# Performance work log

Hardware: AMD Instinct MI355X
Metric: run time of the kernel (lower is better)

## Reference

```python
import jax, jax.numpy as jnp
import numpy as np

NUM_HEADS = 16
HEAD_DIM = 80
DIM = NUM_HEADS * HEAD_DIM
SEQ = 2048
SCALE = HEAD_DIM ** -0.5


def rotate_half(x):
    x1, x2 = jnp.split(x, 2, axis=-1)
    return jnp.concatenate((-x2, x1), axis=-1)


def setup_inputs() -> dict:
    key = jax.random.key(0)
    ks = jax.random.split(key, 8)
    hidden_states = jax.random.normal(ks[0], (SEQ, DIM), dtype=jnp.float32)
    cu_seqlens = jnp.array([0, SEQ], dtype=jnp.int32)  # unused by the math
    # rotary embeddings for head_dim
    inv_freq = 1.0 / (10000.0 ** (jnp.arange(0, HEAD_DIM // 2, dtype=jnp.float32) / (HEAD_DIM // 2)))
    freqs = jnp.outer(jnp.arange(SEQ, dtype=jnp.float32), inv_freq)  # [S, hd/2]
    emb = jnp.concatenate((freqs, freqs), axis=-1)  # [S, hd]
    cos = jnp.cos(emb)
    sin = jnp.sin(emb)
    w_qkv = jax.random.normal(ks[1], (3 * DIM, DIM), dtype=jnp.float32) * (DIM ** -0.5)
    b_qkv = jax.random.normal(ks[2], (3 * DIM,), dtype=jnp.float32) * 0.02
    w_proj = jax.random.normal(ks[3], (DIM, DIM), dtype=jnp.float32) * (DIM ** -0.5)
    b_proj = jax.random.normal(ks[4], (DIM,), dtype=jnp.float32) * 0.02
    return {"hidden_states": hidden_states, "cu_seqlens": cu_seqlens, "cos": cos,
            "sin": sin, "w_qkv": w_qkv, "b_qkv": b_qkv, "w_proj": w_proj, "b_proj": b_proj}


def reference(hidden_states, cu_seqlens, cos, sin, w_qkv, b_qkv, w_proj, b_proj):
    S = hidden_states.shape[0]
    qkv = hidden_states @ w_qkv.T + b_qkv  # [S, 3*D]
    qkv = qkv.reshape(S, 3, NUM_HEADS, HEAD_DIM)
    q, k, v = qkv[:, 0], qkv[:, 1], qkv[:, 2]  # each [S, H, hd]
    c = cos[:, None, :]  # [S, 1, hd]
    s = sin[:, None, :]
    q = q * c + rotate_half(q) * s
    k = k * c + rotate_half(k) * s
    # SDPA, non-causal: [H, S, S]
    scores = jnp.einsum('shd,thd->hst', q, k) * SCALE
    attn = jax.nn.softmax(scores, axis=-1)
    out = jnp.einsum('hst,thd->shd', attn, v).reshape(S, DIM)
    return out @ w_proj.T + b_proj
```

## Files before the change

kernel.cpp:

```cpp
#include <hip/hip_runtime.h>


#define SEQLEN   2048
#define DIMM     1280
#define NHEADS   16
#define HD       80
#define HDP      96
#define QKV_N    3840
#define NSPLIT   4
#define KVSPAN   (SEQLEN / NSPLIT)
#define QSCALE_LOG2E 0.16130083587064776f

#define KSTRIDE  104
#define VFSTRIDE 24

#define EXP2F(x) __builtin_amdgcn_exp2f(x)

#define GLD16(gptr, lptr)                                                      \
    __builtin_amdgcn_global_load_lds(                                          \
        (const __attribute__((address_space(1))) void*)(gptr),                 \
        (__attribute__((address_space(3))) void*)(lptr), 16, 0, 0)

typedef float f32x4 __attribute__((ext_vector_type(4)));
typedef _Float16 half8 __attribute__((ext_vector_type(8)));
typedef _Float16 half4 __attribute__((ext_vector_type(4)));

static __device__ __forceinline__ f32x4 mfma_16x16x32(half8 a, half8 b, f32x4 c) {
    return __builtin_amdgcn_mfma_f32_16x16x32_f16(a, b, c, 0, 0, 0);
}
static __device__ __forceinline__ f32x4 mfma_16x16x16(half4 a, half4 b, f32x4 c) {
    return __builtin_amdgcn_mfma_f32_16x16x16f16(a, b, c, 0, 0, 0);
}
static __device__ __forceinline__ half4 lo4(half8 v) {
    return __builtin_shufflevector(v, v, 0, 1, 2, 3);
}
static __device__ __forceinline__ half4 hi4(half8 v) {
    return __builtin_shufflevector(v, v, 4, 5, 6, 7);
}

__global__ __launch_bounds__(256)
void cast_all(const float* __restrict__ hs, const float* __restrict__ wq,
              const float* __restrict__ wp, _Float16* __restrict__ dhs,
              _Float16* __restrict__ dwq, _Float16* __restrict__ dwp) {
    const int n1 = SEQLEN * DIMM / 4, n2 = QKV_N * DIMM / 4, n3 = DIMM * DIMM / 4;
    int i = blockIdx.x * 256 + threadIdx.x;
    const float4* src; half4* dst; int j;
    if (i < n1)           { src = (const float4*)hs; dst = (half4*)dhs; j = i; }
    else if (i < n1 + n2) { src = (const float4*)wq; dst = (half4*)dwq; j = i - n1; }
    else if (i < n1 + n2 + n3) { src = (const float4*)wp; dst = (half4*)dwp; j = i - n1 - n2; }
    else return;
    const float4 v = src[j];
    half4 h;
    h.x = (_Float16)v.x; h.y = (_Float16)v.y;
    h.z = (_Float16)v.z; h.w = (_Float16)v.w;
    dst[j] = h;
}

template<bool OUT_F16>
__global__ __launch_bounds__(256, 2)
void gemm_bt64(const _Float16* __restrict__ A, const _Float16* __restrict__ B,
               const float* __restrict__ bias, void* __restrict__ Cout,
               int M, int N, int K) {
    __shared__ __align__(16) _Float16 As[2][64 * 32];
    __shared__ __align__(16) _Float16 Bs[2][128 * 32];
    const int tid  = threadIdx.x;
    const int lane = tid & 63;
    const int wave = tid >> 6;
    const int l15  = lane & 15;
    const int quad = lane >> 4;
    const int wm   = wave & 1;
    const int wn   = wave >> 1;
    const long bm = blockIdx.x, bn = blockIdx.y;

    const _Float16* Ag = A + bm * 64 * (long)K;
    const _Float16* Bg = B + bn * 128 * (long)K;

    const int srow = lane >> 2;
    const int scol = (lane & 3) * 8;
    f32x4 acc[2][4] = {};

    for (int k0 = 0; k0 < K; k0 += 64) {
        __syncthreads();
#pragma unroll
        for (int p = 0; p < 2; p++) {
            const int kp = k0 + p * 32;
            const long arow = 16 * wave + srow;
            GLD16(Ag + arow * K + kp + scol, &As[p][512 * wave + lane * 8]);
#pragma unroll
            for (int cc = 0; cc < 2; cc++) {
                const int c = wave + cc * 4;
                const long brow = 16 * c + srow;
                GLD16(Bg + brow * K + kp + scol, &Bs[p][512 * c + lane * 8]);
            }
        }
        __syncthreads();
#pragma unroll
        for (int p = 0; p < 2; p++) {
            half8 af[2], bf[4];
#pragma unroll
            for (int t = 0; t < 2; t++)
                af[t] = *(const half8*)&As[p][(wm * 32 + t * 16 + l15) * 32 + quad * 8];
#pragma unroll
            for (int t = 0; t < 4; t++)
                bf[t] = *(const half8*)&Bs[p][(wn * 64 + t * 16 + l15) * 32 + quad * 8];
#pragma unroll
            for (int mt = 0; mt < 2; mt++)
#pragma unroll
                for (int nt = 0; nt < 4; nt++)
                    acc[mt][nt] = mfma_16x16x32(af[mt], bf[nt], acc[mt][nt]);
        }
    }

    float bv[4];
#pragma unroll
    for (int nt = 0; nt < 4; nt++)
        bv[nt] = bias[bn * 128 + wn * 64 + nt * 16 + l15];

#pragma unroll
    for (int mt = 0; mt < 2; mt++) {
#pragma unroll
        for (int r = 0; r < 4; r++) {
            const long row = bm * 64 + wm * 32 + mt * 16 + quad * 4 + r;
#pragma unroll
            for (int nt = 0; nt < 4; nt++) {
                const long col = bn * 128 + wn * 64 + nt * 16 + l15;
                const float v = acc[mt][nt][r] + bv[nt];
                if (OUT_F16) ((_Float16*)Cout)[row * (long)N + col] = (_Float16)v;
                else         ((float*)Cout)[row * (long)N + col] = v;
            }
        }
    }
}

__global__ __launch_bounds__(256)
void rope_repack_t(const _Float16* __restrict__ qkv,
                   const float* __restrict__ cosb,
                   const float* __restrict__ sinb,
                   _Float16* __restrict__ Qh,
                   _Float16* __restrict__ Kh,
                   _Float16* __restrict__ Vt) {
    const int s0 = blockIdx.x * 64;
    const int h  = blockIdx.y;
    __shared__ __align__(16) _Float16 Ts[64 * 88];
    const int tid = threadIdx.x;

    for (int i = tid; i < 640; i += 256) {
        const int r = i / 10, c = (i - r * 10) * 8;
        *(half8*)&Ts[r * 88 + c] =
            *(const half8*)&qkv[(long)(s0 + r) * QKV_N + 2 * DIMM + h * HD + c];
    }

    for (int i = tid; i < 320; i += 256) {
        const int r = i / 5, d = (i - r * 5) * 8;
        const _Float16* row = qkv + (long)(s0 + r) * QKV_N + h * HD;
        const half8 q0 = *(const half8*)&row[d];
        const half8 q1 = *(const half8*)&row[d + 40];
        const half8 k0 = *(const half8*)&row[DIMM + d];
        const half8 k1 = *(const half8*)&row[DIMM + d + 40];
        const float4 cA = *(const float4*)&cosb[(s0 + r) * HD + d];
        const float4 cB = *(const float4*)&cosb[(s0 + r) * HD + d + 4];
        const float4 sA = *(const float4*)&sinb[(s0 + r) * HD + d];
        const float4 sB = *(const float4*)&sinb[(s0 + r) * HD + d + 4];
        half8 qo0, qo1, ko0, ko1;
#pragma unroll
        for (int j = 0; j < 8; j++) {
            const float cj = (j < 4) ? cA[j] : cB[j - 4];
            const float sj = (j < 4) ? sA[j] : sB[j - 4];
            qo0[j] = (_Float16)(((float)q0[j] * cj - (float)q1[j] * sj) * QSCALE_LOG2E);
            qo1[j] = (_Float16)(((float)q1[j] * cj + (float)q0[j] * sj) * QSCALE_LOG2E);
            ko0[j] = (_Float16)((float)k0[j] * cj - (float)k1[j] * sj);
            ko1[j] = (_Float16)((float)k1[j] * cj + (float)k0[j] * sj);
        }
        const long o = ((long)h * SEQLEN + s0 + r) * HDP;
        *(half8*)&Qh[o + d]      = qo0;
        *(half8*)&Qh[o + d + 40] = qo1;
        *(half8*)&Kh[o + d]      = ko0;
        *(half8*)&Kh[o + d + 40] = ko1;
    }
    for (int i = tid; i < 128; i += 256) {
        const int r = i >> 1, off = HD + (i & 1) * 8;
        const long o = ((long)h * SEQLEN + s0 + r) * HDP + off;
        *(half8*)&Qh[o] = (half8)(_Float16)0.f;
        *(half8*)&Kh[o] = (half8)(_Float16)0.f;
    }
    __syncthreads();
    for (int i = tid; i < 640; i += 256) {
        const int d = i >> 3, sc = (i & 7) * 8;
        half8 v;
#pragma unroll
        for (int j = 0; j < 8; j++) v[j] = Ts[(sc + j) * 88 + d];
        *(half8*)&Vt[((long)h * HD + d) * SEQLEN + s0 + sc] = v;
    }
}

__global__ __launch_bounds__(512, 8)
void attn_kernel(const _Float16* __restrict__ Qh, const _Float16* __restrict__ Kh,
                 const _Float16* __restrict__ Vt,
                 _Float16* __restrict__ Ohat0, _Float16* __restrict__ Ohat1,
                 float* __restrict__ Lpart) {
    const int s0 = blockIdx.x * 128;
    const int h  = blockIdx.y;
    const int z  = blockIdx.z;
    __shared__ __align__(16) _Float16 Ks[64 * KSTRIDE];
    __shared__ __align__(16) _Float16 VF[5 * 64 * VFSTRIDE];

    const int tid  = threadIdx.x;
    const int lane = tid & 63;
    const int wave = tid >> 6;
    const int l15  = lane & 15;
    const int quad = lane >> 4;

    const _Float16* Qg = Qh + ((long)h * SEQLEN + s0 + wave * 16 + l15) * HDP;
    half8 qf[3];
#pragma unroll
    for (int kk = 0; kk < 3; kk++)
        qf[kk] = *(const half8*)&Qg[kk * 32 + quad * 8];

    f32x4 oaccT[5] = {};
    float l_acc = 0.f;

    for (int t0 = z * KVSPAN; t0 < (z + 1) * KVSPAN; t0 += 64) {
        __syncthreads();
        const _Float16* Kg = Kh + ((long)h * SEQLEN + t0) * HDP;
        for (int i = tid; i < 768; i += 512) {
            const int r = i / 12, c = (i - r * 12) * 8;
            *(half8*)&Ks[r * KSTRIDE + c] = *(const half8*)&Kg[(long)r * HDP + c];
        }
        const _Float16* Vtg = Vt + (long)h * HD * SEQLEN + t0;
        for (int i = tid; i < 640; i += 512) {
            const int d = i >> 3, c = (i & 7) * 8;
            const half8 v = *(const half8*)&Vtg[(long)d * SEQLEN + c];
            const int nt = d >> 4, ld = d & 15;
            const int ct = c >> 4, qb = (c & 15) >> 2;
            *(half4*)&VF[(nt * 64 + qb * 16 + ld) * VFSTRIDE + ct * 4]       = lo4(v);
            *(half4*)&VF[(nt * 64 + (qb + 1) * 16 + ld) * VFSTRIDE + ct * 4] = hi4(v);
        }
        __syncthreads();

        f32x4 sa[4] = {};
#pragma unroll
        for (int kk = 0; kk < 3; kk++)
#pragma unroll
            for (int ct = 0; ct < 4; ct++) {
                half8 kf = *(const half8*)&Ks[(ct * 16 + l15) * KSTRIDE + kk * 32 + quad * 8];
                sa[ct] = mfma_16x16x32(kf, qf[kk], sa[ct]);
            }

        half4 pb[4];
#pragma unroll
        for (int ct = 0; ct < 4; ct++)
#pragma unroll
            for (int r = 0; r < 4; r++) {
                const float p = EXP2F(sa[ct][r]);
                l_acc += p;
                pb[ct][r] = (_Float16)p;
            }

#pragma unroll
        for (int nt = 0; nt < 5; nt++) {
            const half8 va = *(const half8*)&VF[(nt * 64 + lane) * VFSTRIDE];
            const half8 vb = *(const half8*)&VF[(nt * 64 + lane) * VFSTRIDE + 8];
            oaccT[nt] = mfma_16x16x16(lo4(va), pb[0], oaccT[nt]);
            oaccT[nt] = mfma_16x16x16(hi4(va), pb[1], oaccT[nt]);
            oaccT[nt] = mfma_16x16x16(lo4(vb), pb[2], oaccT[nt]);
            oaccT[nt] = mfma_16x16x16(hi4(vb), pb[3], oaccT[nt]);
        }
    }

    l_acc += __shfl_xor(l_acc, 16);
    l_acc += __shfl_xor(l_acc, 32);
    const float inv = 1.0f / l_acc;

    _Float16* Oz = (z < 2) ? Ohat0 : Ohat1;
    const long obase = ((long)(z & 1) * NHEADS + h) * SEQLEN;
    const long lbase = ((long)z * NHEADS + h) * SEQLEN;
    const long row = s0 + wave * 16 + l15;
#pragma unroll
    for (int nt = 0; nt < 5; nt++) {
        half4 o;
#pragma unroll
        for (int r = 0; r < 4; r++) o[r] = (_Float16)(oaccT[nt][r] * inv);
        *(half4*)&Oz[(obase + row) * HD + nt * 16 + quad * 4] = o;
    }
    if (quad == 0)
        Lpart[lbase + row] = l_acc;
}

__global__ __launch_bounds__(256)
void attn_combine(const _Float16* __restrict__ Ohat0,
                  const _Float16* __restrict__ Ohat1,
                  const float* __restrict__ Lp,
                  _Float16* __restrict__ attnb) {
    const int i = blockIdx.x * 256 + threadIdx.x;
    if (i >= SEQLEN * DIMM / 4) return;
    const int flat = i * 4;
    const int s = flat / DIMM;
    const int rem = flat - s * DIMM;
    const int h = rem / HD;
    const int d = rem - h * HD;
    float l[NSPLIT], lsum = 0.f;
#pragma unroll
    for (int zi = 0; zi < NSPLIT; zi++) {
        l[zi] = Lp[((long)zi * NHEADS + h) * SEQLEN + s];
        lsum += l[zi];
    }
    const float invl = 1.0f / lsum;
    float acc[4] = {0.f, 0.f, 0.f, 0.f};
#pragma unroll
    for (int zi = 0; zi < NSPLIT; zi++) {
        const _Float16* Oz = (zi < 2) ? Ohat0 : Ohat1;
        const long obase = ((long)(zi & 1) * NHEADS + h) * SEQLEN;
        const half4 o = *(const half4*)&Oz[(obase + s) * HD + d];
        const float w = l[zi] * invl;
#pragma unroll
        for (int j = 0; j < 4; j++) acc[j] += (float)o[j] * w;
    }
    half4 o;
#pragma unroll
    for (int j = 0; j < 4; j++) o[j] = (_Float16)acc[j];
    *(half4*)&attnb[(long)s * DIMM + rem] = o;
}

extern "C" void kernel_launch(void* const* d_in, const int* in_sizes, int n_in,
                              void* d_out, int out_size, void* d_ws, size_t ws_size,
                              hipStream_t stream) {
    const float* hs     = (const float*)d_in[0];
    const float* cosb   = (const float*)d_in[2];
    const float* sinb   = (const float*)d_in[3];
    const float* w_qkv  = (const float*)d_in[4];
    const float* b_qkv  = (const float*)d_in[5];
    const float* w_proj = (const float*)d_in[6];
    const float* b_proj = (const float*)d_in[7];
    float* out = (float*)d_out;

    _Float16* hsb    = (_Float16*)d_ws;
    _Float16* wqkvb  = hsb    + (long)SEQLEN * DIMM;
    _Float16* wprojb = wqkvb  + (long)QKV_N * DIMM;
    _Float16* qkv    = wprojb + (long)DIMM * DIMM;
    _Float16* Qh     = qkv    + (long)SEQLEN * QKV_N;
    _Float16* Kh     = Qh     + (long)NHEADS * SEQLEN * HDP;
    _Float16* Vtb    = Kh     + (long)NHEADS * SEQLEN * HDP;
    _Float16* attnb  = Vtb    + (long)NHEADS * HD * SEQLEN;

    _Float16* Ohat0  = (_Float16*)d_ws;
    float*    LpartB = (float*)(Ohat0 + (long)2 * NHEADS * SEQLEN * HD);
    _Float16* Ohat1  = qkv;

    {
        const int ntot = (SEQLEN * DIMM + QKV_N * DIMM + DIMM * DIMM) / 4;
        cast_all<<<(ntot + 255) / 256, 256, 0, stream>>>(
            hs, w_qkv, w_proj, hsb, wqkvb, wprojb);
    }

    gemm_bt64<true><<<dim3(SEQLEN / 64, QKV_N / 128), 256, 0, stream>>>(
        hsb, wqkvb, b_qkv, qkv, SEQLEN, QKV_N, DIMM);

    rope_repack_t<<<dim3(SEQLEN / 64, NHEADS), 256, 0, stream>>>(
        qkv, cosb, sinb, Qh, Kh, Vtb);

    attn_kernel<<<dim3(SEQLEN / 128, NHEADS, NSPLIT), 512, 0, stream>>>(
        Qh, Kh, Vtb, Ohat0, Ohat1, LpartB);

    attn_combine<<<(SEQLEN * DIMM / 4 + 255) / 256, 256, 0, stream>>>(
        Ohat0, Ohat1, LpartB, attnb);

    gemm_bt64<false><<<dim3(SEQLEN / 64, DIMM / 128), 256, 0, stream>>>(
        attnb, wprojb, b_proj, out, SEQLEN, DIMM, DIMM);
}
```

Before: 206.5 us.

## Register-prefetch K/V tiles, use 16x16x32 MFMA for PV via permlane swaps

Restructures the attention inner loop so the next K and V tiles are loaded from global memory into registers while the current tile is being computed, with each thread given a fixed load assignment. V is now stored in plain row-major shared memory instead of a pre-swizzled fragment layout. The P·V product switches from eight 16x16x16 MFMAs to four 16x16x32 MFMAs per output tile, with P fragments rearranged across lanes using permlane32/16 swaps and packed conversion. The change also adds s_setprio around the MFMA sections and lowers launch bounds occupancy from 8 to 6, trading extra registers for fewer instructions and hidden load latency.

New measurement: 224.8 us. 1.09x slower.

```diff
diff --git a/kernel.cpp b/kernel.cpp
--- a/kernel.cpp
+++ b/kernel.cpp
@@ -12,7 +12,8 @@
 #define QSCALE_LOG2E 0.16130083587064776f
 
 #define KSTRIDE  104
-#define VFSTRIDE 24
+#define VSTRIDE  72
+#define VSOFF    (64 * KSTRIDE)
 
 #define EXP2F(x) __builtin_amdgcn_exp2f(x)
 
@@ -24,18 +25,10 @@
 typedef float f32x4 __attribute__((ext_vector_type(4)));
 typedef _Float16 half8 __attribute__((ext_vector_type(8)));
 typedef _Float16 half4 __attribute__((ext_vector_type(4)));
+typedef int int4v __attribute__((ext_vector_type(4)));
 
 static __device__ __forceinline__ f32x4 mfma_16x16x32(half8 a, half8 b, f32x4 c) {
     return __builtin_amdgcn_mfma_f32_16x16x32_f16(a, b, c, 0, 0, 0);
-}
-static __device__ __forceinline__ f32x4 mfma_16x16x16(half4 a, half4 b, f32x4 c) {
-    return __builtin_amdgcn_mfma_f32_16x16x16f16(a, b, c, 0, 0, 0);
-}
-static __device__ __forceinline__ half4 lo4(half8 v) {
-    return __builtin_shufflevector(v, v, 0, 1, 2, 3);
-}
-static __device__ __forceinline__ half4 hi4(half8 v) {
-    return __builtin_shufflevector(v, v, 4, 5, 6, 7);
 }
 
 __global__ __launch_bounds__(256)
@@ -193,7 +186,7 @@
     }
 }
 
-__global__ __launch_bounds__(512, 8)
+__global__ __launch_bounds__(512, 6)
 void attn_kernel(const _Float16* __restrict__ Qh, const _Float16* __restrict__ Kh,
                  const _Float16* __restrict__ Vt,
                  _Float16* __restrict__ Ohat0, _Float16* __restrict__ Ohat1,
@@ -201,8 +194,7 @@
     const int s0 = blockIdx.x * 128;
     const int h  = blockIdx.y;
     const int z  = blockIdx.z;
-    __shared__ __align__(16) _Float16 Ks[64 * KSTRIDE];
-    __shared__ __align__(16) _Float16 VF[5 * 64 * VFSTRIDE];
+    __shared__ __align__(16) _Float16 Sb[VSOFF + 80 * VSTRIDE];
 
     const int tid  = threadIdx.x;
     const int lane = tid & 63;
@@ -210,61 +202,97 @@
     const int l15  = lane & 15;
     const int quad = lane >> 4;
 
+    const int zBeg = z * KVSPAN, zEnd = zBeg + KVSPAN;
+
     const _Float16* Qg = Qh + ((long)h * SEQLEN + s0 + wave * 16 + l15) * HDP;
     half8 qf[3];
 #pragma unroll
     for (int kk = 0; kk < 3; kk++)
         qf[kk] = *(const half8*)&Qg[kk * 32 + quad * 8];
 
+    const _Float16* p0; const _Float16* p1; const _Float16* p2;
+    int adv1, loff0, loff1, loff2;
+    {
+        const int r0 = tid / 12, c0 = tid - r0 * 12;
+        p0 = Kh + ((long)h * SEQLEN + zBeg + r0) * HDP + c0 * 8;
+        loff0 = r0 * KSTRIDE + c0 * 8;
+        if (tid < 256) {
+            const int r1 = (tid + 512) / 12, c1 = (tid + 512) - r1 * 12;
+            p1 = Kh + ((long)h * SEQLEN + zBeg + r1) * HDP + c1 * 8;
+            adv1 = 64 * HDP;
+            loff1 = r1 * KSTRIDE + c1 * 8;
+        } else {
+            const int v = tid - 256, d = v >> 3, c = v & 7;
+            p1 = Vt + ((long)h * HD + d) * SEQLEN + zBeg + c * 8;
+            adv1 = 64;
+            loff1 = VSOFF + d * VSTRIDE + c * 8;
+        }
+        const int v2 = tid + 256, d2 = v2 >> 3, c2 = v2 & 7;
+        p2 = Vt + ((long)h * HD + d2) * SEQLEN + zBeg + c2 * 8;
+        loff2 = VSOFF + d2 * VSTRIDE + c2 * 8;
+    }
+
+    half8 rg0, rg1, rg2;
+    rg0 = *(const half8*)p0; p0 += 64 * HDP;
+    rg1 = *(const half8*)p1; p1 += adv1;
+    if (tid < 384) { rg2 = *(const half8*)p2; p2 += 64; }
+
     f32x4 oaccT[5] = {};
     float l_acc = 0.f;
 
-    for (int t0 = z * KVSPAN; t0 < (z + 1) * KVSPAN; t0 += 64) {
+    for (int t0 = zBeg; t0 < zEnd; t0 += 64) {
         __syncthreads();
-        const _Float16* Kg = Kh + ((long)h * SEQLEN + t0) * HDP;
-        for (int i = tid; i < 768; i += 512) {
-            const int r = i / 12, c = (i - r * 12) * 8;
-            *(half8*)&Ks[r * KSTRIDE + c] = *(const half8*)&Kg[(long)r * HDP + c];
-        }
-        const _Float16* Vtg = Vt + (long)h * HD * SEQLEN + t0;
-        for (int i = tid; i < 640; i += 512) {
-            const int d = i >> 3, c = (i & 7) * 8;
-            const half8 v = *(const half8*)&Vtg[(long)d * SEQLEN + c];
-            const int nt = d >> 4, ld = d & 15;
-            const int ct = c >> 4, qb = (c & 15) >> 2;
-            *(half4*)&VF[(nt * 64 + qb * 16 + ld) * VFSTRIDE + ct * 4]       = lo4(v);
-            *(half4*)&VF[(nt * 64 + (qb + 1) * 16 + ld) * VFSTRIDE + ct * 4] = hi4(v);
+        *(half8*)&Sb[loff0] = rg0;
+        *(half8*)&Sb[loff1] = rg1;
+        if (tid < 384) *(half8*)&Sb[loff2] = rg2;
+        if (t0 + 64 < zEnd) {
+            rg0 = *(const half8*)p0; p0 += 64 * HDP;
+            rg1 = *(const half8*)p1; p1 += adv1;
+            if (tid < 384) { rg2 = *(const half8*)p2; p2 += 64; }
         }
         __syncthreads();
 
         f32x4 sa[4] = {};
+        __builtin_amdgcn_s_setprio(1);
 #pragma unroll
         for (int kk = 0; kk < 3; kk++)
 #pragma unroll
             for (int ct = 0; ct < 4; ct++) {
-                half8 kf = *(const half8*)&Ks[(ct * 16 + l15) * KSTRIDE + kk * 32 + quad * 8];
+                const half8 kf = *(const half8*)&Sb[(ct * 16 + l15) * KSTRIDE + kk * 32 + quad * 8];
                 sa[ct] = mfma_16x16x32(kf, qf[kk], sa[ct]);
             }
-
-        half4 pb[4];
-#pragma unroll
-        for (int ct = 0; ct < 4; ct++)
-#pragma unroll
-            for (int r = 0; r < 4; r++) {
-                const float p = EXP2F(sa[ct][r]);
-                l_acc += p;
-                pb[ct][r] = (_Float16)p;
-            }
-
+        __builtin_amdgcn_s_setprio(0);
+
+        half8 Bf[2];
+#pragma unroll
+        for (int pr = 0; pr < 2; pr++) {
+            const f32x4 sA = sa[2 * pr], sB = sa[2 * pr + 1];
+            const float eA0 = EXP2F(sA[0]), eA1 = EXP2F(sA[1]);
+            const float eA2 = EXP2F(sA[2]), eA3 = EXP2F(sA[3]);
+            const float eB0 = EXP2F(sB[0]), eB1 = EXP2F(sB[1]);
+            const float eB2 = EXP2F(sB[2]), eB3 = EXP2F(sB[3]);
+            l_acc += ((eA0 + eA1) + (eA2 + eA3)) + ((eB0 + eB1) + (eB2 + eB3));
+            int x0 = __builtin_bit_cast(int, __builtin_amdgcn_cvt_pkrtz(eA0, eA1));
+            int x1 = __builtin_bit_cast(int, __builtin_amdgcn_cvt_pkrtz(eA2, eA3));
+            int y0 = __builtin_bit_cast(int, __builtin_amdgcn_cvt_pkrtz(eB0, eB1));
+            int y1 = __builtin_bit_cast(int, __builtin_amdgcn_cvt_pkrtz(eB2, eB3));
+            asm("v_permlane32_swap_b32 %0, %1" : "+v"(x0), "+v"(y0));
+            asm("v_permlane16_swap_b32 %0, %1" : "+v"(x0), "+v"(y0));
+            asm("v_permlane32_swap_b32 %0, %1" : "+v"(x1), "+v"(y1));
+            asm("v_permlane16_swap_b32 %0, %1" : "+v"(x1), "+v"(y1));
+            const int4v bi = {x0, x1, y0, y1};
+            Bf[pr] = __builtin_bit_cast(half8, bi);
+        }
+
+        __builtin_amdgcn_s_setprio(1);
 #pragma unroll
         for (int nt = 0; nt < 5; nt++) {
-            const half8 va = *(const half8*)&VF[(nt * 64 + lane) * VFSTRIDE];
-            const half8 vb = *(const half8*)&VF[(nt * 64 + lane) * VFSTRIDE + 8];
-            oaccT[nt] = mfma_16x16x16(lo4(va), pb[0], oaccT[nt]);
-            oaccT[nt] = mfma_16x16x16(hi4(va), pb[1], oaccT[nt]);
-            oaccT[nt] = mfma_16x16x16(lo4(vb), pb[2], oaccT[nt]);
-            oaccT[nt] = mfma_16x16x16(hi4(vb), pb[3], oaccT[nt]);
-        }
+            const half8 va0 = *(const half8*)&Sb[VSOFF + (nt * 16 + l15) * VSTRIDE + quad * 8];
+            const half8 va1 = *(const half8*)&Sb[VSOFF + (nt * 16 + l15) * VSTRIDE + 32 + quad * 8];
+            oaccT[nt] = mfma_16x16x32(va0, Bf[0], oaccT[nt]);
+            oaccT[nt] = mfma_16x16x32(va1, Bf[1], oaccT[nt]);
+        }
+        __builtin_amdgcn_s_setprio(0);
     }
 
     l_acc += __shfl_xor(l_acc, 16);
```

## Drop head-dim padding, prefetch K/V tiles into registers, pack softmax sums

Applied to the files above, without the earlier changes.

Q and K are now stored with the true head dimension of 80 instead of padding to 96, and the zero-fill of the padding is removed. The QK product uses two 16x16x32 MFMAs plus one 16x16x16 MFMA per tile, which skips the padded zero columns. K and V tile global loads are issued into registers before the barrier, with precomputed per-thread offsets, so the loads overlap the previous iteration. The exp results are packed with cvt_pkrtz and summed with fdot2, and s_setprio is raised around the MFMA sections. Round-toward-zero packing changes rounding slightly, and holding the prefetched data in registers adds register pressure.

Result: faster. 200.4 us (-2.9%).

```diff
diff --git a/kernel.cpp b/kernel.cpp
--- a/kernel.cpp
+++ b/kernel.cpp
@@ -5,13 +5,12 @@
 #define DIMM     1280
 #define NHEADS   16
 #define HD       80
-#define HDP      96
 #define QKV_N    3840
 #define NSPLIT   4
 #define KVSPAN   (SEQLEN / NSPLIT)
 #define QSCALE_LOG2E 0.16130083587064776f
 
-#define KSTRIDE  104
+#define KSTRIDE  88
 #define VFSTRIDE 24
 
 #define EXP2F(x) __builtin_amdgcn_exp2f(x)
@@ -24,6 +23,7 @@
 typedef float f32x4 __attribute__((ext_vector_type(4)));
 typedef _Float16 half8 __attribute__((ext_vector_type(8)));
 typedef _Float16 half4 __attribute__((ext_vector_type(4)));
+typedef _Float16 half2v __attribute__((ext_vector_type(2)));
 
 static __device__ __forceinline__ f32x4 mfma_16x16x32(half8 a, half8 b, f32x4 c) {
     return __builtin_amdgcn_mfma_f32_16x16x32_f16(a, b, c, 0, 0, 0);
@@ -171,17 +171,11 @@
             ko0[j] = (_Float16)((float)k0[j] * cj - (float)k1[j] * sj);
             ko1[j] = (_Float16)((float)k1[j] * cj + (float)k0[j] * sj);
         }
-        const long o = ((long)h * SEQLEN + s0 + r) * HDP;
+        const long o = ((long)h * SEQLEN + s0 + r) * HD;
         *(half8*)&Qh[o + d]      = qo0;
         *(half8*)&Qh[o + d + 40] = qo1;
         *(half8*)&Kh[o + d]      = ko0;
         *(half8*)&Kh[o + d + 40] = ko1;
-    }
-    for (int i = tid; i < 128; i += 256) {
-        const int r = i >> 1, off = HD + (i & 1) * 8;
-        const long o = ((long)h * SEQLEN + s0 + r) * HDP + off;
-        *(half8*)&Qh[o] = (half8)(_Float16)0.f;
-        *(half8*)&Kh[o] = (half8)(_Float16)0.f;
     }
     __syncthreads();
     for (int i = tid; i < 640; i += 256) {
@@ -210,52 +204,97 @@
     const int l15  = lane & 15;
     const int quad = lane >> 4;
 
-    const _Float16* Qg = Qh + ((long)h * SEQLEN + s0 + wave * 16 + l15) * HDP;
-    half8 qf[3];
-#pragma unroll
-    for (int kk = 0; kk < 3; kk++)
-        qf[kk] = *(const half8*)&Qg[kk * 32 + quad * 8];
+    const int zBeg = z * KVSPAN, zEnd = zBeg + KVSPAN;
+
+    const _Float16* Qg = Qh + ((long)h * SEQLEN + s0 + wave * 16 + l15) * HD;
+    const half8 qf0 = *(const half8*)&Qg[quad * 8];
+    const half8 qf1 = *(const half8*)&Qg[32 + quad * 8];
+    const half4 qf2 = *(const half4*)&Qg[64 + quad * 4];
+
+    int offA, lA, offB, lB0, lB1 = 0, offC = 0, lC0 = 0, lC1 = 0;
+    {
+        const int rA = tid / 10, cA = (tid - rA * 10) * 8;
+        offA = rA * HD + cA;
+        lA   = rA * KSTRIDE + cA;
+        if (tid < 128) {
+            const int cB = tid + 512;
+            const int rB = cB / 10, ccB = (cB - rB * 10) * 8;
+            offB = rB * HD + ccB;
+            lB0  = rB * KSTRIDE + ccB;
+        } else {
+            const int v = tid - 128, d = v >> 3, c8 = (v & 7) * 8;
+            offB = d * SEQLEN + c8;
+            const int nt = d >> 4, ld = d & 15, ct = c8 >> 4, qb = (c8 & 15) >> 2;
+            lB0 = (nt * 64 + qb * 16 + ld) * VFSTRIDE + ct * 4;
+            lB1 = (nt * 64 + (qb + 1) * 16 + ld) * VFSTRIDE + ct * 4;
+        }
+        if (tid < 256) {
+            const int v = tid + 384, d = v >> 3, c8 = (v & 7) * 8;
+            offC = d * SEQLEN + c8;
+            const int nt = d >> 4, ld = d & 15, ct = c8 >> 4, qb = (c8 & 15) >> 2;
+            lC0 = (nt * 64 + qb * 16 + ld) * VFSTRIDE + ct * 4;
+            lC1 = (nt * 64 + (qb + 1) * 16 + ld) * VFSTRIDE + ct * 4;
+        }
+    }
+    const _Float16* KzBase = Kh + ((long)h * SEQLEN + zBeg) * HD;
+    const _Float16* VzBase = Vt + (long)h * HD * SEQLEN + zBeg;
 
     f32x4 oaccT[5] = {};
-    float l_acc = 0.f;
-
-    for (int t0 = z * KVSPAN; t0 < (z + 1) * KVSPAN; t0 += 64) {
+    float la0 = 0.f, la1 = 0.f;
+    const half2v ones2 = {(_Float16)1.f, (_Float16)1.f};
+
+    for (int t0 = zBeg; t0 < zEnd; t0 += 64) {
+        const _Float16* KzT = KzBase + (long)(t0 - zBeg) * HD;
+        const _Float16* VzT = VzBase + (t0 - zBeg);
+        const half8 a = *(const half8*)(KzT + offA);
+        half8 b;
+        if (tid < 128) b = *(const half8*)(KzT + offB);
+        else           b = *(const half8*)(VzT + offB);
+        half8 cv = {};
+        if (tid < 256) cv = *(const half8*)(VzT + offC);
+
         __syncthreads();
-        const _Float16* Kg = Kh + ((long)h * SEQLEN + t0) * HDP;
-        for (int i = tid; i < 768; i += 512) {
-            const int r = i / 12, c = (i - r * 12) * 8;
-            *(half8*)&Ks[r * KSTRIDE + c] = *(const half8*)&Kg[(long)r * HDP + c];
-        }
-        const _Float16* Vtg = Vt + (long)h * HD * SEQLEN + t0;
-        for (int i = tid; i < 640; i += 512) {
-            const int d = i >> 3, c = (i & 7) * 8;
-            const half8 v = *(const half8*)&Vtg[(long)d * SEQLEN + c];
-            const int nt = d >> 4, ld = d & 15;
-            const int ct = c >> 4, qb = (c & 15) >> 2;
-            *(half4*)&VF[(nt * 64 + qb * 16 + ld) * VFSTRIDE + ct * 4]       = lo4(v);
-            *(half4*)&VF[(nt * 64 + (qb + 1) * 16 + ld) * VFSTRIDE + ct * 4] = hi4(v);
+        *(half8*)&Ks[lA] = a;
+        if (tid < 128) { *(half8*)&Ks[lB0] = b; }
+        else {
+            *(half4*)&VF[lB0] = lo4(b);
+            *(half4*)&VF[lB1] = hi4(b);
+        }
+        if (tid < 256) {
+            *(half4*)&VF[lC0] = lo4(cv);
+            *(half4*)&VF[lC1] = hi4(cv);
         }
         __syncthreads();
 
         f32x4 sa[4] = {};
-#pragma unroll
-        for (int kk = 0; kk < 3; kk++)
-#pragma unroll
-            for (int ct = 0; ct < 4; ct++) {
-                half8 kf = *(const half8*)&Ks[(ct * 16 + l15) * KSTRIDE + kk * 32 + quad * 8];
-                sa[ct] = mfma_16x16x32(kf, qf[kk], sa[ct]);
-            }
+        __builtin_amdgcn_s_setprio(1);
+#pragma unroll
+        for (int ct = 0; ct < 4; ct++) {
+            const int kb = (ct * 16 + l15) * KSTRIDE;
+            const half8 kf0 = *(const half8*)&Ks[kb + quad * 8];
+            const half8 kf1 = *(const half8*)&Ks[kb + 32 + quad * 8];
+            sa[ct] = mfma_16x16x32(kf0, qf0, sa[ct]);
+            sa[ct] = mfma_16x16x32(kf1, qf1, sa[ct]);
+            const half4 kf2 = *(const half4*)&Ks[kb + 64 + quad * 4];
+            sa[ct] = mfma_16x16x16(kf2, qf2, sa[ct]);
+        }
+        __builtin_amdgcn_s_setprio(0);
 
         half4 pb[4];
 #pragma unroll
-        for (int ct = 0; ct < 4; ct++)
-#pragma unroll
-            for (int r = 0; r < 4; r++) {
-                const float p = EXP2F(sa[ct][r]);
-                l_acc += p;
-                pb[ct][r] = (_Float16)p;
-            }
-
+        for (int ct = 0; ct < 4; ct++) {
+            const float e0 = EXP2F(sa[ct][0]);
+            const float e1 = EXP2F(sa[ct][1]);
+            const float e2 = EXP2F(sa[ct][2]);
+            const float e3 = EXP2F(sa[ct][3]);
+            const half2v p01 = __builtin_bit_cast(half2v, __builtin_amdgcn_cvt_pkrtz(e0, e1));
+            const half2v p23 = __builtin_bit_cast(half2v, __builtin_amdgcn_cvt_pkrtz(e2, e3));
+            la0 = __builtin_amdgcn_fdot2(p01, ones2, la0, false);
+            la1 = __builtin_amdgcn_fdot2(p23, ones2, la1, false);
+            pb[ct] = __builtin_shufflevector(p01, p23, 0, 1, 2, 3);
+        }
+
+        __builtin_amdgcn_s_setprio(1);
 #pragma unroll
         for (int nt = 0; nt < 5; nt++) {
             const half8 va = *(const half8*)&VF[(nt * 64 + lane) * VFSTRIDE];
@@ -265,8 +304,10 @@
             oaccT[nt] = mfma_16x16x16(lo4(vb), pb[2], oaccT[nt]);
             oaccT[nt] = mfma_16x16x16(hi4(vb), pb[3], oaccT[nt]);
         }
-    }
-
+        __builtin_amdgcn_s_setprio(0);
+    }
+
+    float l_acc = la0 + la1;
     l_acc += __shfl_xor(l_acc, 16);
     l_acc += __shfl_xor(l_acc, 32);
     const float inv = 1.0f / l_acc;
@@ -338,8 +379,8 @@
     _Float16* wprojb = wqkvb  + (long)QKV_N * DIMM;
     _Float16* qkv    = wprojb + (long)DIMM * DIMM;
     _Float16* Qh     = qkv    + (long)SEQLEN * QKV_N;
-    _Float16* Kh     = Qh     + (long)NHEADS * SEQLEN * HDP;
-    _Float16* Vtb    = Kh     + (long)NHEADS * SEQLEN * HDP;
+    _Float16* Kh     = Qh     + (long)NHEADS * SEQLEN * HD;
+    _Float16* Vtb    = Kh     + (long)NHEADS * SEQLEN * HD;
     _Float16* attnb  = Vtb    + (long)NHEADS * HD * SEQLEN;
 
     _Float16* Ohat0  = (_Float16*)d_ws;
```
